# Kernel optimization log

Measured on AMD Instinct MI355X. Metric: run time of the kernel, lower is better.

Reference implementation:

```python
import jax, jax.numpy as jnp
import numpy as np

H, DK, DIM, DFF, DEPTH = 8, 64, 512, 2048, 8
B, LS, LT, VOCAB = 16, 128, 128, 32000


def setup_inputs() -> dict:
    key = jax.random.key(0)
    ks = jax.random.split(key, 20)
    w = lambda k, s: jax.random.normal(k, s, jnp.float32) * 0.02
    N_enc, N_dec = B * LS, B * LT
    base_s = np.arange(B) * LS
    base_t = np.arange(B) * LT
    i = np.arange(LS)
    j = np.arange(LT)
    # encoder self-attn: full bipartite within each sentence
    ee_src = (base_s[:, None, None] + i[None, :, None] + 0 * i[None, None, :]).reshape(-1)
    ee_dst = (base_s[:, None, None] + 0 * i[None, :, None] + i[None, None, :]).reshape(-1)
    # decoder self-attn: causal (key pos <= query pos)
    ii, jj = np.meshgrid(j, j, indexing='ij')  # ii = dst(query) pos, jj = src(key) pos
    m = jj <= ii
    dd_src = (base_t[:, None] + jj[m][None, :]).reshape(-1)
    dd_dst = (base_t[:, None] + ii[m][None, :]).reshape(-1)
    # cross-attn: enc node -> dec node, full within sentence
    ed_src = (base_s[:, None, None] + i[None, :, None] + 0 * j[None, None, :]).reshape(-1)
    ed_dst = (base_t[:, None, None] + 0 * i[None, :, None] + j[None, None, :]).reshape(-1)
    return {
        'emb_src': w(ks[0], (VOCAB, DIM)), 'emb_tgt': w(ks[1], (VOCAB, DIM)),
        'pos_emb': w(ks[2], (LS, DIM)), 'time_emb': w(ks[3], (DEPTH, DIM)),
        'Wqkv_e': w(ks[4], (DIM, 3 * DIM)), 'Wo_e': w(ks[5], (DIM, DIM)),
        'W1_e': w(ks[6], (DIM, DFF)), 'W2_e': w(ks[7], (DFF, DIM)),
        'Wqkv_d': w(ks[8], (DIM, 3 * DIM)), 'Wo_d': w(ks[9], (DIM, DIM)),
        'W1_d': w(ks[10], (DIM, DFF)), 'W2_d': w(ks[11], (DFF, DIM)),
        'Wq_x': w(ks[12], (DIM, DIM)), 'Wkv_x': w(ks[13], (DIM, 2 * DIM)),
        'Wo_x': w(ks[14], (DIM, DIM)), 'Wgen': w(ks[15], (DIM, VOCAB)),
        'src_tokens': jax.random.randint(ks[16], (N_enc,), 0, VOCAB, jnp.int32),
        'tgt_tokens': jax.random.randint(ks[17], (N_dec,), 0, VOCAB, jnp.int32),
        'src_pos': jnp.tile(jnp.arange(LS, dtype=jnp.int32), B),
        'tgt_pos': jnp.tile(jnp.arange(LT, dtype=jnp.int32), B),
        'ee_src': jnp.asarray(ee_src, jnp.int32), 'ee_dst': jnp.asarray(ee_dst, jnp.int32),
        'dd_src': jnp.asarray(dd_src, jnp.int32), 'dd_dst': jnp.asarray(dd_dst, jnp.int32),
        'ed_src': jnp.asarray(ed_src, jnp.int32), 'ed_dst': jnp.asarray(ed_dst, jnp.int32),
    }


def _ln(x):
    m = x.mean(-1, keepdims=True)
    v = ((x - m) ** 2).mean(-1, keepdims=True)
    return (x - m) * jax.lax.rsqrt(v + 1e-5)


def _attn(q, k, v, src, dst, n_dst):
    # q: [Nq,H,DK] (dst side), k/v: [Nk,H,DK] (src side); edge lists [E]
    # src_dot_dst -> scaled_exp -> scatter-sum (src_mul_edge + sum, copy_edge + sum), then wv/z
    s = jnp.exp(jnp.einsum('ehd,ehd->eh', k[src], q[dst]) / np.float32(np.sqrt(DK)))  # [E,H]
    wv = jax.ops.segment_sum(s[:, :, None] * v[src], dst, num_segments=n_dst)  # [Nq,H,DK]
    z = jax.ops.segment_sum(s, dst, num_segments=n_dst)  # [Nq,H]
    return (wv / (z[:, :, None] + 1e-9)).reshape(n_dst, DIM)


def reference(emb_src, emb_tgt, pos_emb, time_emb, Wqkv_e, Wo_e, W1_e, W2_e,
              Wqkv_d, Wo_d, W1_d, W2_d, Wq_x, Wkv_x, Wo_x, Wgen,
              src_tokens, tgt_tokens, src_pos, tgt_pos,
              ee_src, ee_dst, dd_src, dd_dst, ed_src, ed_dst):
    Ne, Nd = src_tokens.shape[0], tgt_tokens.shape[0]
    x_e = emb_src[src_tokens] + pos_emb[src_pos]
    x_d = emb_tgt[tgt_tokens] + pos_emb[tgt_pos]
    # encoder: MAX_DEPTH shared-weight iterations with time+pos enc re-added each step
    for t in range(DEPTH):
        xp = x_e + pos_emb[src_pos] + time_emb[t]
        q, k, v = jnp.split(xp @ Wqkv_e, 3, axis=-1)
        o = _attn(q.reshape(Ne, H, DK), k.reshape(Ne, H, DK), v.reshape(Ne, H, DK), ee_src, ee_dst, Ne)
        x_e = _ln(x_e + o @ Wo_e)
        x_e = _ln(x_e + jax.nn.relu(x_e @ W1_e) @ W2_e)
    # decoder: self-attn (causal dd) then cross-attn (ed) each iteration
    for t in range(DEPTH):
        xp = x_d + pos_emb[tgt_pos] + time_emb[t]
        q, k, v = jnp.split(xp @ Wqkv_d, 3, axis=-1)
        o = _attn(q.reshape(Nd, H, DK), k.reshape(Nd, H, DK), v.reshape(Nd, H, DK), dd_src, dd_dst, Nd)
        x_d = _ln(x_d + o @ Wo_d)
        qx = ((x_d + pos_emb[tgt_pos] + time_emb[t]) @ Wq_x).reshape(Nd, H, DK)
        kx, vx = jnp.split(x_e @ Wkv_x, 2, axis=-1)
        o = _attn(qx, kx.reshape(Ne, H, DK), vx.reshape(Ne, H, DK), ed_src, ed_dst, Nd)
        x_d = _ln(x_d + o @ Wo_x)
        x_d = _ln(x_d + jax.nn.relu(x_d @ W1_d) @ W2_d)
    return jax.nn.log_softmax(x_d @ Wgen, axis=-1)  # generator over dec nodes
```

## Files before the change

### kernel.cpp

```cpp
#include <hip/hip_runtime.h>
#include <hip/hip_bf16.h>
#include <math.h>

#define H 8
#define DK 64
#define DIM 512
#define DFF 2048
#define DEPTH 8
#define VOCAB 32000
#define NTOK 2048

typedef float f32x4 __attribute__((ext_vector_type(4)));
typedef short bf16x8 __attribute__((ext_vector_type(8)));

static __device__ __forceinline__ unsigned short f2bf(float f) {
    unsigned u = __float_as_uint(f);
    return (unsigned short)((u + 0x7FFFu + ((u >> 16) & 1u)) >> 16);
}

#define GLL(src, dst) __builtin_amdgcn_global_load_lds( \
    (const __attribute__((address_space(1))) unsigned int*)(src), \
    (__attribute__((address_space(3))) unsigned int*)(dst), 16, 0, 0)

__global__ void embed_kernel(const float* __restrict__ emb, const int* __restrict__ tok,
                             const float* __restrict__ pos, const int* __restrict__ pidx,
                             float* __restrict__ out, int n4) {
    int idx = blockIdx.x * blockDim.x + threadIdx.x;
    if (idx >= n4) return;
    int i = idx >> 7, d = idx & 127;
    float4 a = ((const float4*)emb)[(size_t)tok[i] * 128 + d];
    float4 b = ((const float4*)pos)[(size_t)pidx[i] * 128 + d];
    ((float4*)out)[idx] = make_float4(a.x + b.x, a.y + b.y, a.z + b.z, a.w + b.w);
}

struct WD { const float* src; unsigned short* dst; int K; int N; int t0; int pad; };
struct WTab { WD d[12]; };

__global__ __launch_bounds__(256) void wconv_all(WTab tab) {
    __shared__ float t[32][33];
    const int bid = blockIdx.x;
    int w = 0;
#pragma unroll
    for (int i = 1; i < 12; i++) if (bid >= tab.d[i].t0) w = i;
    const float* W = tab.d[w].src;
    unsigned short* Wt = tab.d[w].dst;
    const int K = tab.d[w].K, N = tab.d[w].N;
    const int lt = bid - tab.d[w].t0;
    const int txc = N >> 5;
    const int n0 = (lt % txc) << 5, k0 = (lt / txc) << 5;
    const int tid = threadIdx.x;
    const int tx = tid & 31, ty = tid >> 5;
#pragma unroll
    for (int i = 0; i < 32; i += 8)
        t[ty + i][tx] = W[(size_t)(k0 + ty + i) * N + n0 + tx];
    __syncthreads();
#pragma unroll
    for (int i = 0; i < 32; i += 8)
        Wt[(size_t)(n0 + ty + i) * K + k0 + tx] = f2bf(t[tx][ty + i]);
}

template<int EPI>
__global__ __launch_bounds__(256) void gemm_u(
    const float* __restrict__ Af,
    const unsigned short* __restrict__ Bt,
    unsigned short* __restrict__ Cb,
    int M, int N, int K)
{
    __shared__ __align__(16) unsigned short Asm[128 * 64];
    __shared__ __align__(16) unsigned short Bsm[128 * 64];
    const int tid = threadIdx.x;
    const int lane = tid & 63, wid = tid >> 6;
    const int m0 = blockIdx.y * 128, n0 = blockIdx.x * 128;
    const int wm = (wid >> 1) * 64, wn = (wid & 1) * 64;

    f32x4 acc[4][4];
#pragma unroll
    for (int i = 0; i < 4; i++)
#pragma unroll
        for (int j = 0; j < 4; j++) acc[i][j] = (f32x4){0.f, 0.f, 0.f, 0.f};

    for (int k0 = 0; k0 < K; k0 += 64) {
        if (k0) __syncthreads();
#pragma unroll
        for (int it = 0; it < 4; it++) {
            int q = (wid * 4 + it) * 64 + lane;
            int row = q >> 3;
            int cs = (q & 7) ^ (row & 7);
            GLL(Bt + (size_t)(n0 + row) * K + k0 + cs * 8, &Bsm[(wid * 4 + it) * 512]);
        }
#pragma unroll
        for (int it = 0; it < 4; it++) {
            int q = (wid * 4 + it) * 64 + lane;
            int row = q >> 3;
            int cs = q & 7;
            const float* s = Af + (size_t)(m0 + row) * K + k0 + cs * 8;
            float4 u0 = *(const float4*)s, u1 = *(const float4*)(s + 4);
            unsigned short c8[8];
            c8[0] = f2bf(u0.x); c8[1] = f2bf(u0.y); c8[2] = f2bf(u0.z); c8[3] = f2bf(u0.w);
            c8[4] = f2bf(u1.x); c8[5] = f2bf(u1.y); c8[6] = f2bf(u1.z); c8[7] = f2bf(u1.w);
            *(bf16x8*)&Asm[row * 64 + ((cs ^ (row & 7)) * 8)] = *(bf16x8*)c8;
        }
        __syncthreads();
#pragma unroll
        for (int kk = 0; kk < 2; kk++) {
            bf16x8 af[4], bfr[4];
#pragma unroll
            for (int i = 0; i < 4; i++) {
                int rowA = wm + i * 16 + (lane & 15);
                int ca = (kk * 4 + (lane >> 4)) ^ (rowA & 7);
                af[i] = *(const bf16x8*)&Asm[rowA * 64 + ca * 8];
                int rowB = wn + i * 16 + (lane & 15);
                int cb = (kk * 4 + (lane >> 4)) ^ (rowB & 7);
                bfr[i] = *(const bf16x8*)&Bsm[rowB * 64 + cb * 8];
            }
#pragma unroll
            for (int i = 0; i < 4; i++)
#pragma unroll
                for (int j = 0; j < 4; j++)
                    acc[i][j] = __builtin_amdgcn_mfma_f32_16x16x32_bf16(af[i], bfr[j], acc[i][j], 0, 0, 0);
        }
    }
#pragma unroll
    for (int i = 0; i < 4; i++)
#pragma unroll
        for (int j = 0; j < 4; j++)
#pragma unroll
            for (int r = 0; r < 4; r++) {
                int row = m0 + wm + i * 16 + (lane >> 4) * 4 + r;
                int col = n0 + wn + j * 16 + (lane & 15);
                size_t idx = (size_t)row * N + col;
                float v = acc[i][j][r];
                if (EPI == 1) Cb[idx] = f2bf(fmaxf(v, 0.f));
                if (EPI == 3) Cb[idx] = f2bf(v);
            }
}

__global__ __launch_bounds__(256) void gemm_bb(
    const unsigned short* __restrict__ A,
    const unsigned short* __restrict__ Bt,
    const float* __restrict__ R,
    float* __restrict__ Cf,
    int M, int N, int K)
{
    __shared__ __align__(16) unsigned short Asm[64 * 64];
    __shared__ __align__(16) unsigned short Bsm[64 * 64];
    const int tid = threadIdx.x;
    const int lane = tid & 63, wid = tid >> 6;
    const int m0 = blockIdx.y * 64, n0 = blockIdx.x * 64;
    const int wm = (wid >> 1) * 32, wn = (wid & 1) * 32;

    f32x4 acc[2][2];
#pragma unroll
    for (int i = 0; i < 2; i++)
#pragma unroll
        for (int j = 0; j < 2; j++) acc[i][j] = (f32x4){0.f, 0.f, 0.f, 0.f};

    for (int k0 = 0; k0 < K; k0 += 64) {
        if (k0) __syncthreads();
#pragma unroll
        for (int it = 0; it < 2; it++) {
            int q = it * 256 + tid;
            int row = q >> 3;
            int cs = (q & 7) ^ (row & 7);
            GLL(A + (size_t)(m0 + row) * K + k0 + cs * 8, &Asm[(it * 256 + wid * 64) * 8]);
            GLL(Bt + (size_t)(n0 + row) * K + k0 + cs * 8, &Bsm[(it * 256 + wid * 64) * 8]);
        }
        __syncthreads();
#pragma unroll
        for (int kd = 0; kd < 2; kd++) {
            bf16x8 af[2], bfr[2];
#pragma unroll
            for (int i = 0; i < 2; i++) {
                int rowA = wm + i * 16 + (lane & 15);
                int ca = (kd * 4 + (lane >> 4)) ^ (rowA & 7);
                af[i] = *(const bf16x8*)&Asm[rowA * 64 + ca * 8];
                int rowB = wn + i * 16 + (lane & 15);
                int cb = (kd * 4 + (lane >> 4)) ^ (rowB & 7);
                bfr[i] = *(const bf16x8*)&Bsm[rowB * 64 + cb * 8];
            }
#pragma unroll
            for (int i = 0; i < 2; i++)
#pragma unroll
                for (int j = 0; j < 2; j++)
                    acc[i][j] = __builtin_amdgcn_mfma_f32_16x16x32_bf16(af[i], bfr[j], acc[i][j], 0, 0, 0);
        }
    }
#pragma unroll
    for (int i = 0; i < 2; i++)
#pragma unroll
        for (int j = 0; j < 2; j++)
#pragma unroll
            for (int r = 0; r < 4; r++) {
                int row = m0 + wm + i * 16 + (lane >> 4) * 4 + r;
                int col = n0 + wn + j * 16 + (lane & 15);
                size_t idx = (size_t)row * N + col;
                Cf[idx] = acc[i][j][r] + R[idx];
            }
}

__global__ __launch_bounds__(64) void ln_kernel(const float* __restrict__ in,
                                                float* __restrict__ out) {
    const int row = blockIdx.x, lane = threadIdx.x;
    const float* p = in + (size_t)row * DIM;
    float x[8];
#pragma unroll
    for (int i = 0; i < 8; i++) x[i] = p[lane + i * 64];
    float s = 0.f;
#pragma unroll
    for (int i = 0; i < 8; i++) s += x[i];
#pragma unroll
    for (int off = 32; off > 0; off >>= 1) s += __shfl_xor(s, off);
    const float m = s * (1.f / 512.f);
    float v = 0.f;
#pragma unroll
    for (int i = 0; i < 8; i++) { float d = x[i] - m; v += d * d; }
#pragma unroll
    for (int off = 32; off > 0; off >>= 1) v += __shfl_xor(v, off);
    v *= (1.f / 512.f);
    const float inv = 1.f / sqrtf(v + 1e-5f);
    float* q = out + (size_t)row * DIM;
#pragma unroll
    for (int i = 0; i < 8; i++) q[lane + i * 64] = (x[i] - m) * inv;
}

template<int CAUSAL>
static __device__ __forceinline__ void attn_core(
    const unsigned short* Qs, const unsigned short* Ks, const unsigned short* Vt,
    unsigned short* Psw, int wq, int lane, int tok0, int h,
    unsigned short* __restrict__ O)
{
    bf16x8 qa[2][2];
#pragma unroll
    for (int i = 0; i < 2; i++)
#pragma unroll
        for (int kd = 0; kd < 2; kd++) {
            int qr = wq + i * 16 + (lane & 15);
            int ch = (kd * 4 + (lane >> 4)) ^ (qr & 7);
            qa[i][kd] = *(const bf16x8*)&Qs[qr * 64 + ch * 8];
        }

    const int jmax = CAUSAL ? ((wq >> 4) + 2) : 8;
    const int kcmax = CAUSAL ? ((wq >> 5) + 1) : 4;

    float zr[2][4];
#pragma unroll
    for (int i = 0; i < 2; i++)
#pragma unroll
        for (int rr = 0; rr < 4; rr++) zr[i][rr] = 0.f;
    f32x4 oacc[2][4];
#pragma unroll
    for (int i = 0; i < 2; i++)
#pragma unroll
        for (int dt = 0; dt < 4; dt++) oacc[i][dt] = (f32x4){0.f, 0.f, 0.f, 0.f};

    for (int kb = 0; kb < 2; kb++) {
        int j0 = kb * 4;
        if (j0 >= jmax) break;
        int jn = jmax - j0; if (jn > 4) jn = 4;
        f32x4 sacc[2][4];
#pragma unroll
        for (int i = 0; i < 2; i++)
#pragma unroll
            for (int j = 0; j < 4; j++) sacc[i][j] = (f32x4){0.f, 0.f, 0.f, 0.f};
#pragma unroll 2
        for (int kd = 0; kd < 2; kd++) {
            for (int jj = 0; jj < jn; jj++) {
                int kr = (j0 + jj) * 16 + (lane & 15);
                int ch = (kd * 4 + (lane >> 4)) ^ (kr & 7);
                bf16x8 kf = *(const bf16x8*)&Ks[kr * 64 + ch * 8];
                sacc[0][jj] = __builtin_amdgcn_mfma_f32_16x16x32_bf16(qa[0][kd], kf, sacc[0][jj], 0, 0, 0);
                sacc[1][jj] = __builtin_amdgcn_mfma_f32_16x16x32_bf16(qa[1][kd], kf, sacc[1][jj], 0, 0, 0);
            }
        }
#pragma unroll
        for (int i = 0; i < 2; i++) {
            int qbase = wq + i * 16 + (lane >> 4) * 4;
            for (int jj = 0; jj < jn; jj++) {
                int kcol = (j0 + jj) * 16 + (lane & 15);
#pragma unroll
                for (int rr = 0; rr < 4; rr++) {
                    float p = __expf(sacc[i][jj][rr] * 0.125f);
                    if (CAUSAL && kcol > qbase + rr) p = 0.f;
                    zr[i][rr] += p;
                    int prow = i * 16 + (lane >> 4) * 4 + rr;
                    int ch = ((jj * 2 + ((lane & 15) >> 3)) ^ (prow & 7));
                    Psw[prow * 64 + ch * 8 + (lane & 7)] = f2bf(p);
                }
            }
        }
        int kcn = kcmax - kb * 2; if (kcn > 2) kcn = 2;
        for (int kcl = 0; kcl < kcn; kcl++) {
            bf16x8 pa[2];
#pragma unroll
            for (int i = 0; i < 2; i++) {
                int prow = i * 16 + (lane & 15);
                int ch = (kcl * 4 + (lane >> 4)) ^ (prow & 7);
                pa[i] = *(const bf16x8*)&Psw[prow * 64 + ch * 8];
            }
            int kcg = kb * 2 + kcl;
#pragma unroll
            for (int dt = 0; dt < 4; dt++) {
                int d = dt * 16 + (lane & 15);
                bf16x8 vf = *(const bf16x8*)&Vt[d * 132 + (kcg * 4 + (lane >> 4)) * 8];
                oacc[0][dt] = __builtin_amdgcn_mfma_f32_16x16x32_bf16(pa[0], vf, oacc[0][dt], 0, 0, 0);
                oacc[1][dt] = __builtin_amdgcn_mfma_f32_16x16x32_bf16(pa[1], vf, oacc[1][dt], 0, 0, 0);
            }
        }
    }
#pragma unroll
    for (int i = 0; i < 2; i++)
#pragma unroll
        for (int rr = 0; rr < 4; rr++) {
            float z = zr[i][rr];
            z += __shfl_xor(z, 1); z += __shfl_xor(z, 2);
            z += __shfl_xor(z, 4); z += __shfl_xor(z, 8);
            zr[i][rr] = 1.f / (z + 1e-9f);
        }
#pragma unroll
    for (int i = 0; i < 2; i++)
#pragma unroll
        for (int dt = 0; dt < 4; dt++)
#pragma unroll
            for (int rr = 0; rr < 4; rr++) {
                int qrow = tok0 + wq + i * 16 + (lane >> 4) * 4 + rr;
                O[(size_t)qrow * DIM + h * 64 + dt * 16 + (lane & 15)] =
                    f2bf(oacc[i][dt][rr] * zr[i][rr]);
            }
}

template<int CAUSAL>
__global__ __launch_bounds__(256) void fused_attn(
    const float* __restrict__ Xf,
    const float* __restrict__ pos,
    const float* __restrict__ trow,
    const unsigned short* __restrict__ WqkvT,
    unsigned short* __restrict__ O)
{
    __shared__ __align__(16) unsigned short smem[33024];
    unsigned short* Asm = smem;
    unsigned short* Bsm = smem + 8192;
    unsigned short* Qs  = smem;
    unsigned short* Ks  = smem + 8192;
    unsigned short* Vt  = smem + 16384;
    const int tid = threadIdx.x;
    const int lane = tid & 63, wid = tid >> 6;
    unsigned short* Psw = smem + 24832 + wid * 2048;
    const int b = blockIdx.x >> 3, h = blockIdx.x & 7;
    const int tok0 = b * 128;
    const int wq = wid * 32;

    f32x4 acc[2][12];
#pragma unroll
    for (int i = 0; i < 2; i++)
#pragma unroll
        for (int c = 0; c < 12; c++) acc[i][c] = (f32x4){0.f, 0.f, 0.f, 0.f};

    for (int k0 = 0; k0 < 512; k0 += 64) {
        if (k0) __syncthreads();
#pragma unroll
        for (int it = 0; it < 6; it++) {
            int q = it * 256 + tid;
            int r = q >> 3;
            int cs = (q & 7) ^ (r & 7);
            int srow = (r < 64) ? (h * 64 + r)
                     : (r < 128) ? (512 + h * 64 + (r - 64))
                                 : (1024 + h * 64 + (r - 128));
            GLL(WqkvT + (size_t)srow * 512 + k0 + cs * 8, &Bsm[(it * 256 + wid * 64) * 8]);
        }
#pragma unroll
        for (int it = 0; it < 4; it++) {
            int q = (wid * 4 + it) * 64 + lane;
            int row = q >> 3;
            int cs = q & 7;
            const float* s = Xf + (size_t)(tok0 + row) * 512 + k0 + cs * 8;
            const float* pp = pos + (size_t)row * 512 + k0 + cs * 8;
            const float* tt = trow + k0 + cs * 8;
            float4 u0 = *(const float4*)s, u1 = *(const float4*)(s + 4);
            float4 p0 = *(const float4*)pp, p1 = *(const float4*)(pp + 4);
            float4 t0 = *(const float4*)tt, t1 = *(const float4*)(tt + 4);
            u0.x += p0.x + t0.x; u0.y += p0.y + t0.y; u0.z += p0.z + t0.z; u0.w += p0.w + t0.w;
            u1.x += p1.x + t1.x; u1.y += p1.y + t1.y; u1.z += p1.z + t1.z; u1.w += p1.w + t1.w;
            unsigned short c8[8];
            c8[0] = f2bf(u0.x); c8[1] = f2bf(u0.y); c8[2] = f2bf(u0.z); c8[3] = f2bf(u0.w);
            c8[4] = f2bf(u1.x); c8[5] = f2bf(u1.y); c8[6] = f2bf(u1.z); c8[7] = f2bf(u1.w);
            *(bf16x8*)&Asm[row * 64 + ((cs ^ (row & 7)) * 8)] = *(bf16x8*)c8;
        }
        __syncthreads();
#pragma unroll
        for (int kk = 0; kk < 2; kk++) {
            bf16x8 af[2];
#pragma unroll
            for (int i = 0; i < 2; i++) {
                int rowA = wq + i * 16 + (lane & 15);
                int ca = (kk * 4 + (lane >> 4)) ^ (rowA & 7);
                af[i] = *(const bf16x8*)&Asm[rowA * 64 + ca * 8];
            }
#pragma unroll
            for (int c = 0; c < 12; c++) {
                int rowB = c * 16 + (lane & 15);
                int cb = (kk * 4 + (lane >> 4)) ^ (rowB & 7);
                bf16x8 bfr = *(const bf16x8*)&Bsm[rowB * 64 + cb * 8];
                acc[0][c] = __builtin_amdgcn_mfma_f32_16x16x32_bf16(af[0], bfr, acc[0][c], 0, 0, 0);
                acc[1][c] = __builtin_amdgcn_mfma_f32_16x16x32_bf16(af[1], bfr, acc[1][c], 0, 0, 0);
            }
        }
    }
    __syncthreads();
#pragma unroll
    for (int i = 0; i < 2; i++)
#pragma unroll
        for (int c = 0; c < 12; c++)
#pragma unroll
            for (int r = 0; r < 4; r++) {
                int token = wq + i * 16 + (lane >> 4) * 4 + r;
                int col = (c & 3) * 16 + (lane & 15);
                unsigned short v = f2bf(acc[i][c][r]);
                if (c < 4)      Qs[token * 64 + (((col >> 3) ^ (token & 7)) * 8) + (col & 7)] = v;
                else if (c < 8) Ks[token * 64 + (((col >> 3) ^ (token & 7)) * 8) + (col & 7)] = v;
                else            Vt[col * 132 + token] = v;
            }
    __syncthreads();
    attn_core<CAUSAL>(Qs, Ks, Vt, Psw, wq, lane, tok0, h, O);
}

__global__ __launch_bounds__(256) void fused_xattn(
    const float* __restrict__ Xf,
    const float* __restrict__ pos,
    const float* __restrict__ trow,
    const unsigned short* __restrict__ WqT,
    const unsigned short* __restrict__ kvx,
    unsigned short* __restrict__ O)
{
    __shared__ __align__(16) unsigned short smem[33024];
    unsigned short* Asm = smem;
    unsigned short* Bsm = smem + 8192;
    unsigned short* Qs  = smem;
    unsigned short* Ks  = smem + 8192;
    unsigned short* Vt  = smem + 16384;
    const int tid = threadIdx.x;
    const int lane = tid & 63, wid = tid >> 6;
    unsigned short* Psw = smem + 24832 + wid * 2048;
    const int b = blockIdx.x >> 3, h = blockIdx.x & 7;
    const int tok0 = b * 128;
    const int wq = wid * 32;

    f32x4 acc[2][4];
#pragma unroll
    for (int i = 0; i < 2; i++)
#pragma unroll
        for (int c = 0; c < 4; c++) acc[i][c] = (f32x4){0.f, 0.f, 0.f, 0.f};

    for (int k0 = 0; k0 < 512; k0 += 64) {
        if (k0) __syncthreads();
#pragma unroll
        for (int it = 0; it < 2; it++) {
            int q = it * 256 + tid;
            int r = q >> 3;
            int cs = (q & 7) ^ (r & 7);
            GLL(WqT + (size_t)(h * 64 + r) * 512 + k0 + cs * 8, &Bsm[(it * 256 + wid * 64) * 8]);
        }
#pragma unroll
        for (int it = 0; it < 4; it++) {
            int q = (wid * 4 + it) * 64 + lane;
            int row = q >> 3;
            int cs = q & 7;
            const float* s = Xf + (size_t)(tok0 + row) * 512 + k0 + cs * 8;
            const float* pp = pos + (size_t)row * 512 + k0 + cs * 8;
            const float* tt = trow + k0 + cs * 8;
            float4 u0 = *(const float4*)s, u1 = *(const float4*)(s + 4);
            float4 p0 = *(const float4*)pp, p1 = *(const float4*)(pp + 4);
            float4 t0 = *(const float4*)tt, t1 = *(const float4*)(tt + 4);
            u0.x += p0.x + t0.x; u0.y += p0.y + t0.y; u0.z += p0.z + t0.z; u0.w += p0.w + t0.w;
            u1.x += p1.x + t1.x; u1.y += p1.y + t1.y; u1.z += p1.z + t1.z; u1.w += p1.w + t1.w;
            unsigned short c8[8];
            c8[0] = f2bf(u0.x); c8[1] = f2bf(u0.y); c8[2] = f2bf(u0.z); c8[3] = f2bf(u0.w);
            c8[4] = f2bf(u1.x); c8[5] = f2bf(u1.y); c8[6] = f2bf(u1.z); c8[7] = f2bf(u1.w);
            *(bf16x8*)&Asm[row * 64 + ((cs ^ (row & 7)) * 8)] = *(bf16x8*)c8;
        }
        __syncthreads();
#pragma unroll
        for (int kk = 0; kk < 2; kk++) {
            bf16x8 af[2];
#pragma unroll
            for (int i = 0; i < 2; i++) {
                int rowA = wq + i * 16 + (lane & 15);
                int ca = (kk * 4 + (lane >> 4)) ^ (rowA & 7);
                af[i] = *(const bf16x8*)&Asm[rowA * 64 + ca * 8];
            }
#pragma unroll
            for (int c = 0; c < 4; c++) {
                int rowB = c * 16 + (lane & 15);
                int cb = (kk * 4 + (lane >> 4)) ^ (rowB & 7);
                bf16x8 bfr = *(const bf16x8*)&Bsm[rowB * 64 + cb * 8];
                acc[0][c] = __builtin_amdgcn_mfma_f32_16x16x32_bf16(af[0], bfr, acc[0][c], 0, 0, 0);
                acc[1][c] = __builtin_amdgcn_mfma_f32_16x16x32_bf16(af[1], bfr, acc[1][c], 0, 0, 0);
            }
        }
    }
    __syncthreads();
#pragma unroll
    for (int i = 0; i < 2; i++)
#pragma unroll
        for (int c = 0; c < 4; c++)
#pragma unroll
            for (int r = 0; r < 4; r++) {
                int token = wq + i * 16 + (lane >> 4) * 4 + r;
                int col = c * 16 + (lane & 15);
                Qs[token * 64 + (((col >> 3) ^ (token & 7)) * 8) + (col & 7)] = f2bf(acc[i][c][r]);
            }
    {
        int r = tid >> 1, cb = (tid & 1) * 4;
        const unsigned short* Kg = kvx + (size_t)(tok0 + r) * 1024 + h * 64;
        const unsigned short* Vg = Kg + 512;
#pragma unroll
        for (int c = cb; c < cb + 4; c++) {
            bf16x8 kv = *(const bf16x8*)&Kg[c * 8];
            *(bf16x8*)&Ks[r * 64 + ((c ^ (r & 7)) * 8)] = kv;
            bf16x8 vv = *(const bf16x8*)&Vg[c * 8];
#pragma unroll
            for (int j = 0; j < 8; j++)
                Vt[(c * 8 + j) * 132 + r] = (unsigned short)vv[j];
        }
    }
    __syncthreads();
    attn_core<0>(Qs, Ks, Vt, Psw, wq, lane, tok0, h, O);
}

__global__ __launch_bounds__(256) void gemm_gen(
    const float* __restrict__ Af,
    const unsigned short* __restrict__ Bt,
    float* __restrict__ Out,
    float* __restrict__ pm,
    float* __restrict__ psum)
{
    __shared__ __align__(16) unsigned short Asm[128 * 64];
    __shared__ __align__(16) unsigned short Bsm[128 * 64];
    __shared__ float pml[4][64];
    __shared__ float psl[4][64];
    const int tid = threadIdx.x;
    const int lane = tid & 63, wid = tid >> 6;
    const int m0 = blockIdx.x * 128, n0 = blockIdx.y * 128;
    const int wm = (wid >> 1) * 64, wn = (wid & 1) * 64;

    f32x4 acc[4][4];
#pragma unroll
    for (int i = 0; i < 4; i++)
#pragma unroll
        for (int j = 0; j < 4; j++) acc[i][j] = (f32x4){0.f, 0.f, 0.f, 0.f};

    for (int k0 = 0; k0 < 512; k0 += 64) {
        if (k0) __syncthreads();
#pragma unroll
        for (int it = 0; it < 4; it++) {
            int q = (wid * 4 + it) * 64 + lane;
            int row = q >> 3;
            int cs = (q & 7) ^ (row & 7);
            GLL(Bt + (size_t)(n0 + row) * 512 + k0 + cs * 8, &Bsm[(wid * 4 + it) * 512]);
        }
#pragma unroll
        for (int it = 0; it < 4; it++) {
            int q = (wid * 4 + it) * 64 + lane;
            int row = q >> 3;
            int cs = q & 7;
            const float* s = Af + (size_t)(m0 + row) * 512 + k0 + cs * 8;
            float4 u0 = *(const float4*)s, u1 = *(const float4*)(s + 4);
            unsigned short c8[8];
            c8[0] = f2bf(u0.x); c8[1] = f2bf(u0.y); c8[2] = f2bf(u0.z); c8[3] = f2bf(u0.w);
            c8[4] = f2bf(u1.x); c8[5] = f2bf(u1.y); c8[6] = f2bf(u1.z); c8[7] = f2bf(u1.w);
            *(bf16x8*)&Asm[row * 64 + ((cs ^ (row & 7)) * 8)] = *(bf16x8*)c8;
        }
        __syncthreads();
#pragma unroll
        for (int kk = 0; kk < 2; kk++) {
            bf16x8 af[4], bfr[4];
#pragma unroll
            for (int i = 0; i < 4; i++) {
                int rowA = wm + i * 16 + (lane & 15);
                int ca = (kk * 4 + (lane >> 4)) ^ (rowA & 7);
                af[i] = *(const bf16x8*)&Asm[rowA * 64 + ca * 8];
                int rowB = wn + i * 16 + (lane & 15);
                int cb = (kk * 4 + (lane >> 4)) ^ (rowB & 7);
                bfr[i] = *(const bf16x8*)&Bsm[rowB * 64 + cb * 8];
            }
#pragma unroll
            for (int i = 0; i < 4; i++)
#pragma unroll
                for (int j = 0; j < 4; j++)
                    acc[i][j] = __builtin_amdgcn_mfma_f32_16x16x32_bf16(af[i], bfr[j], acc[i][j], 0, 0, 0);
        }
    }
#pragma unroll
    for (int i = 0; i < 4; i++) {
#pragma unroll
        for (int r = 0; r < 4; r++) {
            float mx = fmaxf(fmaxf(acc[i][0][r], acc[i][1][r]),
                             fmaxf(acc[i][2][r], acc[i][3][r]));
            mx = fmaxf(mx, __shfl_xor(mx, 1));
            mx = fmaxf(mx, __shfl_xor(mx, 2));
            mx = fmaxf(mx, __shfl_xor(mx, 4));
            mx = fmaxf(mx, __shfl_xor(mx, 8));
            float s = __expf(acc[i][0][r] - mx) + __expf(acc[i][1][r] - mx) +
                      __expf(acc[i][2][r] - mx) + __expf(acc[i][3][r] - mx);
            s += __shfl_xor(s, 1); s += __shfl_xor(s, 2);
            s += __shfl_xor(s, 4); s += __shfl_xor(s, 8);
            if ((lane & 15) == 0) {
                int li = i * 16 + (lane >> 4) * 4 + r;
                pml[wid][li] = mx;
                psl[wid][li] = s;
            }
        }
    }
    __syncthreads();
    if (tid < 128) {
        int half = tid >> 6, lr = tid & 63;
        int wa = half * 2, wb = half * 2 + 1;
        float ma = pml[wa][lr], mb = pml[wb][lr];
        float m = fmaxf(ma, mb);
        float s = psl[wa][lr] * __expf(ma - m) + psl[wb][lr] * __expf(mb - m);
        pm[(size_t)(m0 + tid) * 256 + blockIdx.y] = m;
        psum[(size_t)(m0 + tid) * 256 + blockIdx.y] = s;
    }
#pragma unroll
    for (int i = 0; i < 4; i++)
#pragma unroll
        for (int j = 0; j < 4; j++)
#pragma unroll
            for (int r = 0; r < 4; r++) {
                int row = m0 + wm + i * 16 + (lane >> 4) * 4 + r;
                int col = n0 + wn + j * 16 + (lane & 15);
                Out[(size_t)row * VOCAB + col] = acc[i][j][r];
            }
}

__global__ __launch_bounds__(64) void lse_kernel(const float* __restrict__ pm,
                                                 const float* __restrict__ psum,
                                                 float* __restrict__ lse) {
    const int row = blockIdx.x, t = threadIdx.x;
    float m = -1e30f, s = 0.f;
    for (int nb = t; nb < 250; nb += 64) {
        float mm = pm[(size_t)row * 256 + nb];
        float ss = psum[(size_t)row * 256 + nb];
        float M = fmaxf(m, mm);
        s = s * __expf(m - M) + ss * __expf(mm - M);
        m = M;
    }
#pragma unroll
    for (int off = 32; off > 0; off >>= 1) {
        float mo = __shfl_xor(m, off), so = __shfl_xor(s, off);
        float M = fmaxf(m, mo);
        s = s * __expf(m - M) + so * __expf(mo - M);
        m = M;
    }
    if (t == 0) lse[row] = m + __logf(s);
}

__global__ __launch_bounds__(256) void sub_kernel(float* __restrict__ out,
                                                  const float* __restrict__ lse) {
    const int row = blockIdx.x;
    const float l = lse[row];
    float4* p = (float4*)(out + (size_t)row * VOCAB);
    for (int i = threadIdx.x; i < VOCAB / 4; i += 256) {
        float4 v = p[i];
        p[i] = make_float4(v.x - l, v.y - l, v.z - l, v.w - l);
    }
}

extern "C" void kernel_launch(void* const* d_in, const int* in_sizes, int n_in,
                              void* d_out, int out_size, void* d_ws, size_t ws_size,
                              hipStream_t stream) {
    const float* emb_src  = (const float*)d_in[0];
    const float* emb_tgt  = (const float*)d_in[1];
    const float* pos_emb  = (const float*)d_in[2];
    const float* time_emb = (const float*)d_in[3];
    const float* Wqkv_e   = (const float*)d_in[4];
    const float* Wo_e     = (const float*)d_in[5];
    const float* W1_e     = (const float*)d_in[6];
    const float* W2_e     = (const float*)d_in[7];
    const float* Wqkv_d   = (const float*)d_in[8];
    const float* Wo_d     = (const float*)d_in[9];
    const float* W1_d     = (const float*)d_in[10];
    const float* W2_d     = (const float*)d_in[11];
    const float* Wq_x     = (const float*)d_in[12];
    const float* Wkv_x    = (const float*)d_in[13];
    const float* Wo_x     = (const float*)d_in[14];
    const float* Wgen     = (const float*)d_in[15];
    const int* src_tokens = (const int*)d_in[16];
    const int* tgt_tokens = (const int*)d_in[17];
    const int* src_pos    = (const int*)d_in[18];
    const int* tgt_pos    = (const int*)d_in[19];

    char* w = (char*)d_ws;
    float* x_e = (float*)(w);
    float* x_d = (float*)(w + (4u << 20));
    float* tmp = (float*)(w + (8u << 20));
    unsigned short* kvx_bf = (unsigned short*)(w + (12u << 20));
    unsigned short* o_bf   = (unsigned short*)(w + (16u << 20));
    unsigned short* hid_bf = (unsigned short*)(w + (18u << 20));
    float* pm   = (float*)(w + (26u << 20));
    float* psum = (float*)(w + (28u << 20));
    float* lse  = (float*)(w + (30u << 20));
    unsigned short* wts    = (unsigned short*)(w + (31u << 20));

    unsigned short* WqkvE_t = wts;
    unsigned short* WoE_t   = WqkvE_t + 786432;
    unsigned short* W1E_t   = WoE_t   + 262144;
    unsigned short* W2E_t   = W1E_t   + 1048576;
    unsigned short* WqkvD_t = W2E_t   + 1048576;
    unsigned short* WoD_t   = WqkvD_t + 786432;
    unsigned short* W1D_t   = WoD_t   + 262144;
    unsigned short* W2D_t   = W1D_t   + 1048576;
    unsigned short* WqX_t   = W2D_t   + 1048576;
    unsigned short* WkvX_t  = WqX_t   + 262144;
    unsigned short* WoX_t   = WkvX_t  + 524288;
    unsigned short* Wgen_t  = WoX_t   + 262144;

    float* out = (float*)d_out;

    WTab tab;
    auto set = [&](int i, const float* s, unsigned short* d, int K, int N, int t0) {
        tab.d[i].src = s; tab.d[i].dst = d; tab.d[i].K = K; tab.d[i].N = N;
        tab.d[i].t0 = t0; tab.d[i].pad = 0;
    };
    set(0,  Wqkv_e, WqkvE_t, 512, 1536, 0);
    set(1,  Wo_e,   WoE_t,   512, 512,  768);
    set(2,  W1_e,   W1E_t,   512, 2048, 1024);
    set(3,  W2_e,   W2E_t,   2048, 512, 2048);
    set(4,  Wqkv_d, WqkvD_t, 512, 1536, 3072);
    set(5,  Wo_d,   WoD_t,   512, 512,  3840);
    set(6,  W1_d,   W1D_t,   512, 2048, 4096);
    set(7,  W2_d,   W2D_t,   2048, 512, 5120);
    set(8,  Wq_x,   WqX_t,   512, 512,  6144);
    set(9,  Wkv_x,  WkvX_t,  512, 1024, 6400);
    set(10, Wo_x,   WoX_t,   512, 512,  6912);
    set(11, Wgen,   Wgen_t,  512, 32000, 7168);
    wconv_all<<<23168, 256, 0, stream>>>(tab);

    const int n4 = NTOK * (DIM / 4);
    dim3 eb(256), eg((n4 + 255) / 256);
    embed_kernel<<<eg, eb, 0, stream>>>(emb_src, src_tokens, pos_emb, src_pos, x_e, n4);
    embed_kernel<<<eg, eb, 0, stream>>>(emb_tgt, tgt_tokens, pos_emb, tgt_pos, x_d, n4);

    const dim3 gFF(DFF / 128, NTOK / 128), gKV(1024 / 128, NTOK / 128),
               g64(512 / 64, NTOK / 64);

    for (int t = 0; t < DEPTH; t++) {
        const float* trow = time_emb + (size_t)t * DIM;
        fused_attn<0><<<128, 256, 0, stream>>>(x_e, pos_emb, trow, WqkvE_t, o_bf);
        gemm_bb<<<g64, 256, 0, stream>>>(o_bf, WoE_t, x_e, tmp, NTOK, 512, 512);
        ln_kernel<<<NTOK, 64, 0, stream>>>(tmp, x_e);
        gemm_u<1><<<gFF, 256, 0, stream>>>(x_e, W1E_t, hid_bf, NTOK, DFF, 512);
        gemm_bb<<<g64, 256, 0, stream>>>(hid_bf, W2E_t, x_e, tmp, NTOK, 512, 2048);
        ln_kernel<<<NTOK, 64, 0, stream>>>(tmp, x_e);
    }

    gemm_u<3><<<gKV, 256, 0, stream>>>(x_e, WkvX_t, kvx_bf, NTOK, 1024, 512);

    for (int t = 0; t < DEPTH; t++) {
        const float* trow = time_emb + (size_t)t * DIM;
        fused_attn<1><<<128, 256, 0, stream>>>(x_d, pos_emb, trow, WqkvD_t, o_bf);
        gemm_bb<<<g64, 256, 0, stream>>>(o_bf, WoD_t, x_d, tmp, NTOK, 512, 512);
        ln_kernel<<<NTOK, 64, 0, stream>>>(tmp, x_d);

        fused_xattn<<<128, 256, 0, stream>>>(x_d, pos_emb, trow, WqX_t, kvx_bf, o_bf);
        gemm_bb<<<g64, 256, 0, stream>>>(o_bf, WoX_t, x_d, tmp, NTOK, 512, 512);
        ln_kernel<<<NTOK, 64, 0, stream>>>(tmp, x_d);

        gemm_u<1><<<gFF, 256, 0, stream>>>(x_d, W1D_t, hid_bf, NTOK, DFF, 512);
        gemm_bb<<<g64, 256, 0, stream>>>(hid_bf, W2D_t, x_d, tmp, NTOK, 512, 2048);
        ln_kernel<<<NTOK, 64, 0, stream>>>(tmp, x_d);
    }

    gemm_gen<<<dim3(16, 250), 256, 0, stream>>>(x_d, Wgen_t, out, pm, psum);
    lse_kernel<<<NTOK, 64, 0, stream>>>(pm, psum, lse);
    sub_kernel<<<NTOK, 256, 0, stream>>>(out, lse);
}
```

Measured before the change: 2.053 ms.

## Emit bf16 copies from layernorm and double attention block waves

Layernorm now writes a bf16 copy of its output alongside the fp32 one. The FFN-up, cross-KV and generator GEMMs then load A directly into LDS with async global-to-LDS loads instead of converting fp32 in-register. The fused attention and cross-attention kernels move from 256 to 512 threads, with each wave handling 16 query rows instead of 32. This raises the number of waves per block for the 128-block grids, at the cost of less register-level reuse of the loaded B fragments and an extra bf16 store per layernorm.

```diff
diff --git a/kernel.cpp b/kernel.cpp
--- a/kernel.cpp
+++ b/kernel.cpp
@@ -60,8 +60,8 @@
 }
 
 template<int EPI>
-__global__ __launch_bounds__(256) void gemm_u(
-    const float* __restrict__ Af,
+__global__ __launch_bounds__(256) void gemm_rb(
+    const unsigned short* __restrict__ A,
     const unsigned short* __restrict__ Bt,
     unsigned short* __restrict__ Cb,
     int M, int N, int K)
@@ -87,18 +87,7 @@
             int row = q >> 3;
             int cs = (q & 7) ^ (row & 7);
             GLL(Bt + (size_t)(n0 + row) * K + k0 + cs * 8, &Bsm[(wid * 4 + it) * 512]);
-        }
-#pragma unroll
-        for (int it = 0; it < 4; it++) {
-            int q = (wid * 4 + it) * 64 + lane;
-            int row = q >> 3;
-            int cs = q & 7;
-            const float* s = Af + (size_t)(m0 + row) * K + k0 + cs * 8;
-            float4 u0 = *(const float4*)s, u1 = *(const float4*)(s + 4);
-            unsigned short c8[8];
-            c8[0] = f2bf(u0.x); c8[1] = f2bf(u0.y); c8[2] = f2bf(u0.z); c8[3] = f2bf(u0.w);
-            c8[4] = f2bf(u1.x); c8[5] = f2bf(u1.y); c8[6] = f2bf(u1.z); c8[7] = f2bf(u1.w);
-            *(bf16x8*)&Asm[row * 64 + ((cs ^ (row & 7)) * 8)] = *(bf16x8*)c8;
+            GLL(A + (size_t)(m0 + row) * K + k0 + cs * 8, &Asm[(wid * 4 + it) * 512]);
         }
         __syncthreads();
 #pragma unroll
@@ -199,7 +188,8 @@
 }
 
 __global__ __launch_bounds__(64) void ln_kernel(const float* __restrict__ in,
-                                                float* __restrict__ out) {
+                                                float* __restrict__ out,
+                                                unsigned short* __restrict__ outb) {
     const int row = blockIdx.x, lane = threadIdx.x;
     const float* p = in + (size_t)row * DIM;
     float x[8];
@@ -219,117 +209,101 @@
     v *= (1.f / 512.f);
     const float inv = 1.f / sqrtf(v + 1e-5f);
     float* q = out + (size_t)row * DIM;
-#pragma unroll
-    for (int i = 0; i < 8; i++) q[lane + i * 64] = (x[i] - m) * inv;
+    unsigned short* qb = outb + (size_t)row * DIM;
+#pragma unroll
+    for (int i = 0; i < 8; i++) {
+        float y = (x[i] - m) * inv;
+        q[lane + i * 64] = y;
+        qb[lane + i * 64] = f2bf(y);
+    }
 }
 
 template<int CAUSAL>
-static __device__ __forceinline__ void attn_core(
+static __device__ __forceinline__ void attn_core16(
     const unsigned short* Qs, const unsigned short* Ks, const unsigned short* Vt,
     unsigned short* Psw, int wq, int lane, int tok0, int h,
     unsigned short* __restrict__ O)
 {
-    bf16x8 qa[2][2];
-#pragma unroll
-    for (int i = 0; i < 2; i++)
-#pragma unroll
-        for (int kd = 0; kd < 2; kd++) {
-            int qr = wq + i * 16 + (lane & 15);
-            int ch = (kd * 4 + (lane >> 4)) ^ (qr & 7);
-            qa[i][kd] = *(const bf16x8*)&Qs[qr * 64 + ch * 8];
-        }
-
-    const int jmax = CAUSAL ? ((wq >> 4) + 2) : 8;
+    bf16x8 qa[2];
+#pragma unroll
+    for (int kd = 0; kd < 2; kd++) {
+        int qr = wq + (lane & 15);
+        int ch = (kd * 4 + (lane >> 4)) ^ (qr & 7);
+        qa[kd] = *(const bf16x8*)&Qs[qr * 64 + ch * 8];
+    }
     const int kcmax = CAUSAL ? ((wq >> 5) + 1) : 4;
-
-    float zr[2][4];
-#pragma unroll
-    for (int i = 0; i < 2; i++)
-#pragma unroll
-        for (int rr = 0; rr < 4; rr++) zr[i][rr] = 0.f;
-    f32x4 oacc[2][4];
-#pragma unroll
-    for (int i = 0; i < 2; i++)
-#pragma unroll
-        for (int dt = 0; dt < 4; dt++) oacc[i][dt] = (f32x4){0.f, 0.f, 0.f, 0.f};
+    const int jmax = CAUSAL ? (kcmax * 2) : 8;
+
+    float zr[4] = {0.f, 0.f, 0.f, 0.f};
+    f32x4 oacc[4];
+#pragma unroll
+    for (int dt = 0; dt < 4; dt++) oacc[dt] = (f32x4){0.f, 0.f, 0.f, 0.f};
 
     for (int kb = 0; kb < 2; kb++) {
         int j0 = kb * 4;
         if (j0 >= jmax) break;
         int jn = jmax - j0; if (jn > 4) jn = 4;
-        f32x4 sacc[2][4];
-#pragma unroll
-        for (int i = 0; i < 2; i++)
-#pragma unroll
-            for (int j = 0; j < 4; j++) sacc[i][j] = (f32x4){0.f, 0.f, 0.f, 0.f};
+        f32x4 sacc[4];
+#pragma unroll
+        for (int j = 0; j < 4; j++) sacc[j] = (f32x4){0.f, 0.f, 0.f, 0.f};
 #pragma unroll 2
         for (int kd = 0; kd < 2; kd++) {
             for (int jj = 0; jj < jn; jj++) {
                 int kr = (j0 + jj) * 16 + (lane & 15);
                 int ch = (kd * 4 + (lane >> 4)) ^ (kr & 7);
                 bf16x8 kf = *(const bf16x8*)&Ks[kr * 64 + ch * 8];
-                sacc[0][jj] = __builtin_amdgcn_mfma_f32_16x16x32_bf16(qa[0][kd], kf, sacc[0][jj], 0, 0, 0);
-                sacc[1][jj] = __builtin_amdgcn_mfma_f32_16x16x32_bf16(qa[1][kd], kf, sacc[1][jj], 0, 0, 0);
-            }
-        }
-#pragma unroll
-        for (int i = 0; i < 2; i++) {
-            int qbase = wq + i * 16 + (lane >> 4) * 4;
-            for (int jj = 0; jj < jn; jj++) {
-                int kcol = (j0 + jj) * 16 + (lane & 15);
-#pragma unroll
-                for (int rr = 0; rr < 4; rr++) {
-                    float p = __expf(sacc[i][jj][rr] * 0.125f);
-                    if (CAUSAL && kcol > qbase + rr) p = 0.f;
-                    zr[i][rr] += p;
-                    int prow = i * 16 + (lane >> 4) * 4 + rr;
-                    int ch = ((jj * 2 + ((lane & 15) >> 3)) ^ (prow & 7));
-                    Psw[prow * 64 + ch * 8 + (lane & 7)] = f2bf(p);
-                }
+                sacc[jj] = __builtin_amdgcn_mfma_f32_16x16x32_bf16(qa[kd], kf, sacc[jj], 0, 0, 0);
+            }
+        }
+        int qbase = wq + (lane >> 4) * 4;
+        for (int jj = 0; jj < jn; jj++) {
+            int kcol = (j0 + jj) * 16 + (lane & 15);
+#pragma unroll
+            for (int rr = 0; rr < 4; rr++) {
+                float p = __expf(sacc[jj][rr] * 0.125f);
+                if (CAUSAL && kcol > qbase + rr) p = 0.f;
+                zr[rr] += p;
+                int prow = (lane >> 4) * 4 + rr;
+                int ch = ((jj * 2 + ((lane & 15) >> 3)) ^ (prow & 7));
+                Psw[prow * 64 + ch * 8 + (lane & 7)] = f2bf(p);
             }
         }
         int kcn = kcmax - kb * 2; if (kcn > 2) kcn = 2;
         for (int kcl = 0; kcl < kcn; kcl++) {
-            bf16x8 pa[2];
-#pragma unroll
-            for (int i = 0; i < 2; i++) {
-                int prow = i * 16 + (lane & 15);
+            bf16x8 pa;
+            {
+                int prow = lane & 15;
                 int ch = (kcl * 4 + (lane >> 4)) ^ (prow & 7);
-                pa[i] = *(const bf16x8*)&Psw[prow * 64 + ch * 8];
+                pa = *(const bf16x8*)&Psw[prow * 64 + ch * 8];
             }
             int kcg = kb * 2 + kcl;
 #pragma unroll
             for (int dt = 0; dt < 4; dt++) {
                 int d = dt * 16 + (lane & 15);
                 bf16x8 vf = *(const bf16x8*)&Vt[d * 132 + (kcg * 4 + (lane >> 4)) * 8];
-                oacc[0][dt] = __builtin_amdgcn_mfma_f32_16x16x32_bf16(pa[0], vf, oacc[0][dt], 0, 0, 0);
-                oacc[1][dt] = __builtin_amdgcn_mfma_f32_16x16x32_bf16(pa[1], vf, oacc[1][dt], 0, 0, 0);
-            }
-        }
-    }
-#pragma unroll
-    for (int i = 0; i < 2; i++)
+                oacc[dt] = __builtin_amdgcn_mfma_f32_16x16x32_bf16(pa, vf, oacc[dt], 0, 0, 0);
+            }
+        }
+    }
+#pragma unroll
+    for (int rr = 0; rr < 4; rr++) {
+        float z = zr[rr];
+        z += __shfl_xor(z, 1); z += __shfl_xor(z, 2);
+        z += __shfl_xor(z, 4); z += __shfl_xor(z, 8);
+        zr[rr] = 1.f / (z + 1e-9f);
+    }
+#pragma unroll
+    for (int dt = 0; dt < 4; dt++)
 #pragma unroll
         for (int rr = 0; rr < 4; rr++) {
-            float z = zr[i][rr];
-            z += __shfl_xor(z, 1); z += __shfl_xor(z, 2);
-            z += __shfl_xor(z, 4); z += __shfl_xor(z, 8);
-            zr[i][rr] = 1.f / (z + 1e-9f);
-        }
-#pragma unroll
-    for (int i = 0; i < 2; i++)
-#pragma unroll
-        for (int dt = 0; dt < 4; dt++)
-#pragma unroll
-            for (int rr = 0; rr < 4; rr++) {
-                int qrow = tok0 + wq + i * 16 + (lane >> 4) * 4 + rr;
-                O[(size_t)qrow * DIM + h * 64 + dt * 16 + (lane & 15)] =
-                    f2bf(oacc[i][dt][rr] * zr[i][rr]);
-            }
+            int qrow = tok0 + wq + (lane >> 4) * 4 + rr;
+            O[(size_t)qrow * DIM + h * 64 + dt * 16 + (lane & 15)] =
+                f2bf(oacc[dt][rr] * zr[rr]);
+        }
 }
 
 template<int CAUSAL>
-__global__ __launch_bounds__(256) void fused_attn(
+__global__ __launch_bounds__(512) void fused_attn(
     const float* __restrict__ Xf,
     const float* __restrict__ pos,
     const float* __restrict__ trow,
@@ -344,32 +318,30 @@
     unsigned short* Vt  = smem + 16384;
     const int tid = threadIdx.x;
     const int lane = tid & 63, wid = tid >> 6;
-    unsigned short* Psw = smem + 24832 + wid * 2048;
+    unsigned short* Psw = smem + 24832 + wid * 1024;
     const int b = blockIdx.x >> 3, h = blockIdx.x & 7;
     const int tok0 = b * 128;
-    const int wq = wid * 32;
-
-    f32x4 acc[2][12];
-#pragma unroll
-    for (int i = 0; i < 2; i++)
-#pragma unroll
-        for (int c = 0; c < 12; c++) acc[i][c] = (f32x4){0.f, 0.f, 0.f, 0.f};
+    const int wq = wid * 16;
+
+    f32x4 acc[12];
+#pragma unroll
+    for (int c = 0; c < 12; c++) acc[c] = (f32x4){0.f, 0.f, 0.f, 0.f};
 
     for (int k0 = 0; k0 < 512; k0 += 64) {
         if (k0) __syncthreads();
 #pragma unroll
-        for (int it = 0; it < 6; it++) {
-            int q = it * 256 + tid;
+        for (int it = 0; it < 3; it++) {
+            int q = it * 512 + wid * 64 + lane;
             int r = q >> 3;
             int cs = (q & 7) ^ (r & 7);
             int srow = (r < 64) ? (h * 64 + r)
                      : (r < 128) ? (512 + h * 64 + (r - 64))
                                  : (1024 + h * 64 + (r - 128));
-            GLL(WqkvT + (size_t)srow * 512 + k0 + cs * 8, &Bsm[(it * 256 + wid * 64) * 8]);
-        }
-#pragma unroll
-        for (int it = 0; it < 4; it++) {
-            int q = (wid * 4 + it) * 64 + lane;
+            GLL(WqkvT + (size_t)srow * 512 + k0 + cs * 8, &Bsm[(it * 512 + wid * 64) * 8]);
+        }
+#pragma unroll
+        for (int it = 0; it < 2; it++) {
+            int q = it * 512 + tid;
             int row = q >> 3;
             int cs = q & 7;
             const float* s = Xf + (size_t)(tok0 + row) * 512 + k0 + cs * 8;
@@ -388,42 +360,35 @@
         __syncthreads();
 #pragma unroll
         for (int kk = 0; kk < 2; kk++) {
-            bf16x8 af[2];
-#pragma unroll
-            for (int i = 0; i < 2; i++) {
-                int rowA = wq + i * 16 + (lane & 15);
-                int ca = (kk * 4 + (lane >> 4)) ^ (rowA & 7);
-                af[i] = *(const bf16x8*)&Asm[rowA * 64 + ca * 8];
-            }
+            int rowA = wq + (lane & 15);
+            int ca = (kk * 4 + (lane >> 4)) ^ (rowA & 7);
+            bf16x8 af = *(const bf16x8*)&Asm[rowA * 64 + ca * 8];
 #pragma unroll
             for (int c = 0; c < 12; c++) {
                 int rowB = c * 16 + (lane & 15);
                 int cb = (kk * 4 + (lane >> 4)) ^ (rowB & 7);
                 bf16x8 bfr = *(const bf16x8*)&Bsm[rowB * 64 + cb * 8];
-                acc[0][c] = __builtin_amdgcn_mfma_f32_16x16x32_bf16(af[0], bfr, acc[0][c], 0, 0, 0);
-                acc[1][c] = __builtin_amdgcn_mfma_f32_16x16x32_bf16(af[1], bfr, acc[1][c], 0, 0, 0);
+                acc[c] = __builtin_amdgcn_mfma_f32_16x16x32_bf16(af, bfr, acc[c], 0, 0, 0);
             }
         }
     }
     __syncthreads();
 #pragma unroll
-    for (int i = 0; i < 2; i++)
-#pragma unroll
-        for (int c = 0; c < 12; c++)
-#pragma unroll
-            for (int r = 0; r < 4; r++) {
-                int token = wq + i * 16 + (lane >> 4) * 4 + r;
-                int col = (c & 3) * 16 + (lane & 15);
-                unsigned short v = f2bf(acc[i][c][r]);
-                if (c < 4)      Qs[token * 64 + (((col >> 3) ^ (token & 7)) * 8) + (col & 7)] = v;
-                else if (c < 8) Ks[token * 64 + (((col >> 3) ^ (token & 7)) * 8) + (col & 7)] = v;
-                else            Vt[col * 132 + token] = v;
-            }
+    for (int c = 0; c < 12; c++)
+#pragma unroll
+        for (int r = 0; r < 4; r++) {
+            int token = wq + (lane >> 4) * 4 + r;
+            int col = (c & 3) * 16 + (lane & 15);
+            unsigned short v = f2bf(acc[c][r]);
+            if (c < 4)      Qs[token * 64 + (((col >> 3) ^ (token & 7)) * 8) + (col & 7)] = v;
+            else if (c < 8) Ks[token * 64 + (((col >> 3) ^ (token & 7)) * 8) + (col & 7)] = v;
+            else            Vt[col * 132 + token] = v;
+        }
     __syncthreads();
-    attn_core<CAUSAL>(Qs, Ks, Vt, Psw, wq, lane, tok0, h, O);
-}
-
-__global__ __launch_bounds__(256) void fused_xattn(
+    attn_core16<CAUSAL>(Qs, Ks, Vt, Psw, wq, lane, tok0, h, O);
+}
+
+__global__ __launch_bounds__(512) void fused_xattn(
     const float* __restrict__ Xf,
     const float* __restrict__ pos,
     const float* __restrict__ trow,
@@ -439,29 +404,26 @@
     unsigned short* Vt  = smem + 16384;
     const int tid = threadIdx.x;
     const int lane = tid & 63, wid = tid >> 6;
-    unsigned short* Psw = smem + 24832 + wid * 2048;
+    unsigned short* Psw = smem + 24832 + wid * 1024;
     const int b = blockIdx.x >> 3, h = blockIdx.x & 7;
     const int tok0 = b * 128;
-    const int wq = wid * 32;
-
-    f32x4 acc[2][4];
-#pragma unroll
-    for (int i = 0; i < 2; i++)
-#pragma unroll
-        for (int c = 0; c < 4; c++) acc[i][c] = (f32x4){0.f, 0.f, 0.f, 0.f};
+    const int wq = wid * 16;
+
+    f32x4 acc[4];
+#pragma unroll
+    for (int c = 0; c < 4; c++) acc[c] = (f32x4){0.f, 0.f, 0.f, 0.f};
 
     for (int k0 = 0; k0 < 512; k0 += 64) {
         if (k0) __syncthreads();
-#pragma unroll
-        for (int it = 0; it < 2; it++) {
-            int q = it * 256 + tid;
+        {
+            int q = wid * 64 + lane;
             int r = q >> 3;
             int cs = (q & 7) ^ (r & 7);
-            GLL(WqT + (size_t)(h * 64 + r) * 512 + k0 + cs * 8, &Bsm[(it * 256 + wid * 64) * 8]);
-        }
-#pragma unroll
-        for (int it = 0; it < 4; it++) {
-            int q = (wid * 4 + it) * 64 + lane;
+            GLL(WqT + (size_t)(h * 64 + r) * 512 + k0 + cs * 8, &Bsm[(wid * 64) * 8]);
+        }
+#pragma unroll
+        for (int it = 0; it < 2; it++) {
+            int q = it * 512 + tid;
             int row = q >> 3;
             int cs = q & 7;
             const float* s = Xf + (size_t)(tok0 + row) * 512 + k0 + cs * 8;
@@ -480,40 +442,33 @@
         __syncthreads();
 #pragma unroll
         for (int kk = 0; kk < 2; kk++) {
-            bf16x8 af[2];
-#pragma unroll
-            for (int i = 0; i < 2; i++) {
-                int rowA = wq + i * 16 + (lane & 15);
-                int ca = (kk * 4 + (lane >> 4)) ^ (rowA & 7);
-                af[i] = *(const bf16x8*)&Asm[rowA * 64 + ca * 8];
-            }
+            int rowA = wq + (lane & 15);
+            int ca = (kk * 4 + (lane >> 4)) ^ (rowA & 7);
+            bf16x8 af = *(const bf16x8*)&Asm[rowA * 64 + ca * 8];
 #pragma unroll
             for (int c = 0; c < 4; c++) {
                 int rowB = c * 16 + (lane & 15);
                 int cb = (kk * 4 + (lane >> 4)) ^ (rowB & 7);
                 bf16x8 bfr = *(const bf16x8*)&Bsm[rowB * 64 + cb * 8];
-                acc[0][c] = __builtin_amdgcn_mfma_f32_16x16x32_bf16(af[0], bfr, acc[0][c], 0, 0, 0);
-                acc[1][c] = __builtin_amdgcn_mfma_f32_16x16x32_bf16(af[1], bfr, acc[1][c], 0, 0, 0);
+                acc[c] = __builtin_amdgcn_mfma_f32_16x16x32_bf16(af, bfr, acc[c], 0, 0, 0);
             }
         }
     }
     __syncthreads();
 #pragma unroll
-    for (int i = 0; i < 2; i++)
-#pragma unroll
-        for (int c = 0; c < 4; c++)
-#pragma unroll
-            for (int r = 0; r < 4; r++) {
-                int token = wq + i * 16 + (lane >> 4) * 4 + r;
-                int col = c * 16 + (lane & 15);
-                Qs[token * 64 + (((col >> 3) ^ (token & 7)) * 8) + (col & 7)] = f2bf(acc[i][c][r]);
-            }
+    for (int c = 0; c < 4; c++)
+#pragma unroll
+        for (int r = 0; r < 4; r++) {
+            int token = wq + (lane >> 4) * 4 + r;
+            int col = c * 16 + (lane & 15);
+            Qs[token * 64 + (((col >> 3) ^ (token & 7)) * 8) + (col & 7)] = f2bf(acc[c][r]);
+        }
     {
-        int r = tid >> 1, cb = (tid & 1) * 4;
+        int r = tid >> 2, c0 = (tid & 3) * 2;
         const unsigned short* Kg = kvx + (size_t)(tok0 + r) * 1024 + h * 64;
         const unsigned short* Vg = Kg + 512;
 #pragma unroll
-        for (int c = cb; c < cb + 4; c++) {
+        for (int c = c0; c < c0 + 2; c++) {
             bf16x8 kv = *(const bf16x8*)&Kg[c * 8];
             *(bf16x8*)&Ks[r * 64 + ((c ^ (r & 7)) * 8)] = kv;
             bf16x8 vv = *(const bf16x8*)&Vg[c * 8];
@@ -523,11 +478,11 @@
         }
     }
     __syncthreads();
-    attn_core<0>(Qs, Ks, Vt, Psw, wq, lane, tok0, h, O);
+    attn_core16<0>(Qs, Ks, Vt, Psw, wq, lane, tok0, h, O);
 }
 
 __global__ __launch_bounds__(256) void gemm_gen(
-    const float* __restrict__ Af,
+    const unsigned short* __restrict__ Ab,
     const unsigned short* __restrict__ Bt,
     float* __restrict__ Out,
     float* __restrict__ pm,
@@ -556,18 +511,7 @@
             int row = q >> 3;
             int cs = (q & 7) ^ (row & 7);
             GLL(Bt + (size_t)(n0 + row) * 512 + k0 + cs * 8, &Bsm[(wid * 4 + it) * 512]);
-        }
-#pragma unroll
-        for (int it = 0; it < 4; it++) {
-            int q = (wid * 4 + it) * 64 + lane;
-            int row = q >> 3;
-            int cs = q & 7;
-            const float* s = Af + (size_t)(m0 + row) * 512 + k0 + cs * 8;
-            float4 u0 = *(const float4*)s, u1 = *(const float4*)(s + 4);
-            unsigned short c8[8];
-            c8[0] = f2bf(u0.x); c8[1] = f2bf(u0.y); c8[2] = f2bf(u0.z); c8[3] = f2bf(u0.w);
-            c8[4] = f2bf(u1.x); c8[5] = f2bf(u1.y); c8[6] = f2bf(u1.z); c8[7] = f2bf(u1.w);
-            *(bf16x8*)&Asm[row * 64 + ((cs ^ (row & 7)) * 8)] = *(bf16x8*)c8;
+            GLL(Ab + (size_t)(m0 + row) * 512 + k0 + cs * 8, &Asm[(wid * 4 + it) * 512]);
         }
         __syncthreads();
 #pragma unroll
@@ -699,7 +643,9 @@
     float* pm   = (float*)(w + (26u << 20));
     float* psum = (float*)(w + (28u << 20));
     float* lse  = (float*)(w + (30u << 20));
-    unsigned short* wts    = (unsigned short*)(w + (31u << 20));
+    unsigned short* xe_bf = (unsigned short*)(w + (31u << 20));
+    unsigned short* xd_bf = (unsigned short*)(w + (33u << 20));
+    unsigned short* wts   = (unsigned short*)(w + (35u << 20));
 
     unsigned short* WqkvE_t = wts;
     unsigned short* WoE_t   = WqkvE_t + 786432;
@@ -745,32 +691,32 @@
 
     for (int t = 0; t < DEPTH; t++) {
         const float* trow = time_emb + (size_t)t * DIM;
-        fused_attn<0><<<128, 256, 0, stream>>>(x_e, pos_emb, trow, WqkvE_t, o_bf);
+        fused_attn<0><<<128, 512, 0, stream>>>(x_e, pos_emb, trow, WqkvE_t, o_bf);
         gemm_bb<<<g64, 256, 0, stream>>>(o_bf, WoE_t, x_e, tmp, NTOK, 512, 512);
-        ln_kernel<<<NTOK, 64, 0, stream>>>(tmp, x_e);
-        gemm_u<1><<<gFF, 256, 0, stream>>>(x_e, W1E_t, hid_bf, NTOK, DFF, 512);
+        ln_kernel<<<NTOK, 64, 0, stream>>>(tmp, x_e, xe_bf);
+        gemm_rb<1><<<gFF, 256, 0, stream>>>(xe_bf, W1E_t, hid_bf, NTOK, DFF, 512);
         gemm_bb<<<g64, 256, 0, stream>>>(hid_bf, W2E_t, x_e, tmp, NTOK, 512, 2048);
-        ln_kernel<<<NTOK, 64, 0, stream>>>(tmp, x_e);
-    }
-
-    gemm_u<3><<<gKV, 256, 0, stream>>>(x_e, WkvX_t, kvx_bf, NTOK, 1024, 512);
+        ln_kernel<<<NTOK, 64, 0, stream>>>(tmp, x_e, xe_bf);
+    }
+
+    gemm_rb<3><<<gKV, 256, 0, stream>>>(xe_bf, WkvX_t, kvx_bf, NTOK, 1024, 512);
 
     for (int t = 0; t < DEPTH; t++) {
         const float* trow = time_emb + (size_t)t * DIM;
-        fused_attn<1><<<128, 256, 0, stream>>>(x_d, pos_emb, trow, WqkvD_t, o_bf);
+        fused_attn<1><<<128, 512, 0, stream>>>(x_d, pos_emb, trow, WqkvD_t, o_bf);
         gemm_bb<<<g64, 256, 0, stream>>>(o_bf, WoD_t, x_d, tmp, NTOK, 512, 512);
-        ln_kernel<<<NTOK, 64, 0, stream>>>(tmp, x_d);
-
-        fused_xattn<<<128, 256, 0, stream>>>(x_d, pos_emb, trow, WqX_t, kvx_bf, o_bf);
+        ln_kernel<<<NTOK, 64, 0, stream>>>(tmp, x_d, xd_bf);
+
+        fused_xattn<<<128, 512, 0, stream>>>(x_d, pos_emb, trow, WqX_t, kvx_bf, o_bf);
         gemm_bb<<<g64, 256, 0, stream>>>(o_bf, WoX_t, x_d, tmp, NTOK, 512, 512);
-        ln_kernel<<<NTOK, 64, 0, stream>>>(tmp, x_d);
-
-        gemm_u<1><<<gFF, 256, 0, stream>>>(x_d, W1D_t, hid_bf, NTOK, DFF, 512);
+        ln_kernel<<<NTOK, 64, 0, stream>>>(tmp, x_d, xd_bf);
+
+        gemm_rb<1><<<gFF, 256, 0, stream>>>(xd_bf, W1D_t, hid_bf, NTOK, DFF, 512);
         gemm_bb<<<g64, 256, 0, stream>>>(hid_bf, W2D_t, x_d, tmp, NTOK, 512, 2048);
-        ln_kernel<<<NTOK, 64, 0, stream>>>(tmp, x_d);
-    }
-
-    gemm_gen<<<dim3(16, 250), 256, 0, stream>>>(x_d, Wgen_t, out, pm, psum);
+        ln_kernel<<<NTOK, 64, 0, stream>>>(tmp, x_d, xd_bf);
+    }
+
+    gemm_gen<<<dim3(16, 250), 256, 0, stream>>>(xd_bf, Wgen_t, out, pm, psum);
     lse_kernel<<<NTOK, 64, 0, stream>>>(pm, psum, lse);
     sub_kernel<<<NTOK, 256, 0, stream>>>(out, lse);
 }
```

Result: faster. 1.855 ms (-9.6%).
